# Optimization experiments

Hardware: AMD Instinct MI355X
Metric: run time of the kernel (lower is better)

## Reference

```python
import jax, jax.numpy as jnp
import numpy as np

B = 262144
G = 21       # number of groups (hardcoded in the torch forward)
GS = 8       # features per group
BASIC = 13   # data[:, :13]
H = 512      # hidden_dim
OUT = 1      # output_size


def setup_inputs() -> dict:
    key = jax.random.key(0)
    k0, k1, k2, k3, k4, k5, k6 = jax.random.split(key, 7)
    data = jax.random.normal(k0, (B, BASIC + G * GS), dtype=jnp.float32)
    # per-group Linear(GS, 1): stacked weights [G, GS] and biases [G]
    gW = jax.random.normal(k1, (G, GS), dtype=jnp.float32) * 0.1
    gb = jax.random.normal(k2, (G,), dtype=jnp.float32) * 0.1
    W1 = jax.random.normal(k3, (BASIC + G, H), dtype=jnp.float32) * 0.1
    b1 = jax.random.normal(k4, (H,), dtype=jnp.float32) * 0.1
    W2 = jax.random.normal(k5, (H, OUT), dtype=jnp.float32) * 0.1
    b2 = jax.random.normal(k6, (OUT,), dtype=jnp.float32) * 0.1
    return {"data": data, "gW": gW, "gb": gb, "W1": W1, "b1": b1, "W2": W2, "b2": b2}


def reference(data, gW, gb, W1, b1, W2, b2):
    # Groups are the contiguous, exclusive column slices 13:181 -> [B, G, GS].
    grouped = data[:, BASIC:].reshape(data.shape[0], G, GS)
    # 21 tiny Linear(GS,1)+Sigmoid ops, fused into one batched contraction.
    gout = jax.nn.sigmoid(jnp.einsum("bgd,gd->bg", grouped, gW) + gb)  # [B, G]
    mixed = jnp.concatenate([data[:, :BASIC], gout], axis=1)           # [B, 13+21]
    h = jax.nn.relu(mixed @ W1 + b1)                                   # [B, H]
    return jax.nn.sigmoid(h @ W2 + b2)                                 # [B, OUT]
```

## Files before the change

kernel.cpp:

```cpp
#include <hip/hip_runtime.h>
#include <hip/hip_bf16.h>


#define B_ROWS 262144
#define DFEAT  181
#define BASICF 13
#define NG     21
#define MIXF   34
#define HID    512
#define NT     512
#define TILE   128
#define ROWS_PER_BLOCK 512
#define NTILES (ROWS_PER_BLOCK / TILE)
#define NBLK   (B_ROWS / ROWS_PER_BLOCK)

typedef __attribute__((ext_vector_type(8))) short short8;
typedef __attribute__((ext_vector_type(4))) float float4_t;

__device__ __forceinline__ short f2bf(float f) {
    union { float f; unsigned u; } v; v.f = f;
    unsigned r = (v.u + 0x7FFFu + ((v.u >> 16) & 1u)) >> 16;
    return (short)r;
}
__device__ __forceinline__ float sigm(float x) { return 1.0f / (1.0f + __expf(-x)); }

__global__ __launch_bounds__(NT, 4) void fused_mfma_kernel(
    const float* __restrict__ data, const float* __restrict__ gW,
    const float* __restrict__ gb, const float* __restrict__ W1,
    const float* __restrict__ b1, const float* __restrict__ W2,
    const float* __restrict__ b2, float* __restrict__ out)
{
    __shared__ __align__(16) short   W1f[32 * 64 * 8];
    __shared__ __align__(16) short   mixed[TILE * 32];
    __shared__ __align__(8)  float   mtail[TILE][2];
    __shared__ __align__(16) float4_t wbt[HID];
    __shared__ float gws[NG * 8];
    __shared__ float gbs[NG];

    const int tid = threadIdx.x;

    #pragma unroll 4
    for (int k = 0; k < 32; ++k) {
        int c = tid;
        int t = c >> 4, ci = c & 15;
        int l = ((k >> 3) << 4) + ci;
        int j = k & 7;
        W1f[(t * 64 + l) * 8 + j] = f2bf(W1[k * HID + c]);
    }
    {
        int c = tid;
        wbt[c] = (float4_t){ b1[c], W2[c], W1[32 * HID + c], W1[33 * HID + c] };
    }
    if (tid < NG * 8) gws[tid] = gW[tid];
    if (tid < NG)     gbs[tid] = gb[tid];
    __syncthreads();

    const int wave = tid >> 6;
    const int lane = tid & 63;
    const int lg   = lane >> 4;
    const int li   = lane & 15;
    const float b2v = b2[0];
    const int blk_row0 = blockIdx.x * ROWS_PER_BLOCK;

    {
        const int row0 = blk_row0;
        for (int it = 0; it < 9; ++it) {
            int u = tid + it * NT;
            if (u < TILE * MIXF) {
                int row = u / MIXF, c = u - row * MIXF;
                const float* dr = data + (size_t)(row0 + row) * DFEAT;
                if (c < BASICF) {
                    mixed[row * 32 + c] = f2bf(dr[c]);
                } else {
                    int g = c - BASICF;
                    const float* x = dr + BASICF + g * 8;
                    float s = gbs[g];
                    #pragma unroll
                    for (int k = 0; k < 8; ++k) s = fmaf(x[k], gws[g * 8 + k], s);
                    float v = sigm(s);
                    if (c < 32) mixed[row * 32 + c] = f2bf(v);
                    else        mtail[row][c - 32] = v;
                }
            }
        }
    }
    __syncthreads();

    for (int tile = 0; tile < NTILES; ++tile) {
        const int trow0 = blk_row0 + tile * TILE;

        short8 a0 = *(const short8*)&mixed[(wave * 16 + li) * 32 + lg * 8];
        float2 mt[4];
        #pragma unroll
        for (int j = 0; j < 4; ++j)
            mt[j] = *(const float2*)&mtail[wave * 16 + lg * 4 + j][0];
        __syncthreads();

        if (tile + 1 < NTILES) {
            const int row0 = trow0 + TILE;
            for (int it = 0; it < 9; ++it) {
                int u = tid + it * NT;
                if (u < TILE * MIXF) {
                    int row = u / MIXF, c = u - row * MIXF;
                    const float* dr = data + (size_t)(row0 + row) * DFEAT;
                    if (c < BASICF) {
                        mixed[row * 32 + c] = f2bf(dr[c]);
                    } else {
                        int g = c - BASICF;
                        const float* x = dr + BASICF + g * 8;
                        float s = gbs[g];
                        #pragma unroll
                        for (int k = 0; k < 8; ++k) s = fmaf(x[k], gws[g * 8 + k], s);
                        float v = sigm(s);
                        if (c < 32) mixed[row * 32 + c] = f2bf(v);
                        else        mtail[row][c - 32] = v;
                    }
                }
            }
        }

        float4_t acc = {0.f, 0.f, 0.f, 0.f};
        for (int t = 0; t < 32; ++t) {
            short8 bf = *(const short8*)&W1f[(t * 64 + lane) * 8];
            float4_t c4 = {0.f, 0.f, 0.f, 0.f};
            c4 = __builtin_amdgcn_mfma_f32_16x16x32_bf16(a0, bf, c4, 0, 0, 0);
            int c = t * 16 + li;
            float4_t wv = wbt[c];
            #pragma unroll
            for (int j = 0; j < 4; ++j) {
                float h = c4[j] + wv.x;
                h = fmaf(mt[j].x, wv.z, h);
                h = fmaf(mt[j].y, wv.w, h);
                h = fmaxf(h, 0.f);
                acc[j] = fmaf(h, wv.y, acc[j]);
            }
        }
        #pragma unroll
        for (int m = 1; m < 16; m <<= 1) {
            #pragma unroll
            for (int j = 0; j < 4; ++j) acc[j] += __shfl_xor(acc[j], m, 64);
        }
        if (li == 0) {
            #pragma unroll
            for (int j = 0; j < 4; ++j)
                out[trow0 + wave * 16 + lg * 4 + j] = sigm(acc[j] + b2v);
        }
        __syncthreads();
    }
}

extern "C" void kernel_launch(void* const* d_in, const int* in_sizes, int n_in,
                              void* d_out, int out_size, void* d_ws, size_t ws_size,
                              hipStream_t stream) {
    (void)in_sizes; (void)n_in; (void)out_size; (void)d_ws; (void)ws_size;
    const float* data = (const float*)d_in[0];
    const float* gW   = (const float*)d_in[1];
    const float* gb   = (const float*)d_in[2];
    const float* W1   = (const float*)d_in[3];
    const float* b1   = (const float*)d_in[4];
    const float* W2   = (const float*)d_in[5];
    const float* b2   = (const float*)d_in[6];
    float* out = (float*)d_out;
    fused_mfma_kernel<<<dim3(NBLK), dim3(NT), 0, stream>>>(data, gW, gb, W1, b1, W2, b2, out);
}
```

Before: 51.66 us.

## Split fused kernel into feature-build and MLP kernels via workspace

Splits the single fused kernel into two. The first computes the bf16 mixed features and the fp32 tail into a global workspace with a grid-stride loop, and the second runs the MFMA MLP reading from that workspace. This removes the per-tile block barriers and the in-kernel producer/consumer staging through shared memory. In exchange it adds a global round trip for the intermediate (about 17 MB written and read) and a second launch, and the MLP blocks each still rebuild the W1 fragment table.

Measured after the change: 96.21 us. 1.86x slower.

```diff
diff --git a/kernel.cpp b/kernel.cpp
--- a/kernel.cpp
+++ b/kernel.cpp
@@ -8,11 +8,6 @@
 #define NG     21
 #define MIXF   34
 #define HID    512
-#define NT     512
-#define TILE   128
-#define ROWS_PER_BLOCK 512
-#define NTILES (ROWS_PER_BLOCK / TILE)
-#define NBLK   (B_ROWS / ROWS_PER_BLOCK)
 
 typedef __attribute__((ext_vector_type(8))) short short8;
 typedef __attribute__((ext_vector_type(4))) float float4_t;
@@ -24,35 +19,59 @@
 }
 __device__ __forceinline__ float sigm(float x) { return 1.0f / (1.0f + __expf(-x)); }
 
-__global__ __launch_bounds__(NT, 4) void fused_mfma_kernel(
+#define BUILD_BLOCKS 2048
+__global__ __launch_bounds__(256) void build_kernel(
     const float* __restrict__ data, const float* __restrict__ gW,
-    const float* __restrict__ gb, const float* __restrict__ W1,
-    const float* __restrict__ b1, const float* __restrict__ W2,
-    const float* __restrict__ b2, float* __restrict__ out)
+    const float* __restrict__ gb, short* __restrict__ mixed_g,
+    float* __restrict__ tail_g)
+{
+    __shared__ float gws[NG * 8];
+    __shared__ float gbs[NG];
+    if (threadIdx.x < NG * 8) gws[threadIdx.x] = gW[threadIdx.x];
+    if (threadIdx.x < NG)     gbs[threadIdx.x] = gb[threadIdx.x];
+    __syncthreads();
+
+    const int total  = B_ROWS * MIXF;
+    const int stride = BUILD_BLOCKS * 256;
+    for (int u = blockIdx.x * 256 + threadIdx.x; u < total; u += stride) {
+        int row = u / MIXF;
+        int c   = u - row * MIXF;
+        const float* dr = data + (size_t)row * DFEAT;
+        if (c < BASICF) {
+            mixed_g[row * 32 + c] = f2bf(dr[c]);
+        } else {
+            int g = c - BASICF;
+            const float* x = dr + BASICF + g * 8;
+            float s = gbs[g];
+            #pragma unroll
+            for (int k = 0; k < 8; ++k) s = fmaf(x[k], gws[g * 8 + k], s);
+            float v = sigm(s);
+            if (c < 32) mixed_g[row * 32 + c] = f2bf(v);
+            else        tail_g[row * 2 + (c - 32)] = v;
+        }
+    }
+}
+
+#define MLP_BLOCKS 1024
+__global__ __launch_bounds__(256) void mlp_kernel(
+    const short* __restrict__ mixed_g, const float* __restrict__ tail_g,
+    const float* __restrict__ W1, const float* __restrict__ b1,
+    const float* __restrict__ W2, const float* __restrict__ b2,
+    float* __restrict__ out)
 {
     __shared__ __align__(16) short   W1f[32 * 64 * 8];
-    __shared__ __align__(16) short   mixed[TILE * 32];
-    __shared__ __align__(8)  float   mtail[TILE][2];
     __shared__ __align__(16) float4_t wbt[HID];
-    __shared__ float gws[NG * 8];
-    __shared__ float gbs[NG];
 
     const int tid = threadIdx.x;
-
-    #pragma unroll 4
-    for (int k = 0; k < 32; ++k) {
-        int c = tid;
+    for (int idx = tid; idx < 32 * HID; idx += 256) {
+        int k = idx >> 9, c = idx & 511;
         int t = c >> 4, ci = c & 15;
         int l = ((k >> 3) << 4) + ci;
         int j = k & 7;
         W1f[(t * 64 + l) * 8 + j] = f2bf(W1[k * HID + c]);
     }
-    {
-        int c = tid;
+    for (int c = tid; c < HID; c += 256)
         wbt[c] = (float4_t){ b1[c], W2[c], W1[32 * HID + c], W1[33 * HID + c] };
-    }
-    if (tid < NG * 8) gws[tid] = gW[tid];
-    if (tid < NG)     gbs[tid] = gb[tid];
     __syncthreads();
 
     const int wave = tid >> 6;
@@ -60,64 +79,17 @@
     const int lg   = lane >> 4;
     const int li   = lane & 15;
     const float b2v = b2[0];
-    const int blk_row0 = blockIdx.x * ROWS_PER_BLOCK;
 
-    {
-        const int row0 = blk_row0;
-        for (int it = 0; it < 9; ++it) {
-            int u = tid + it * NT;
-            if (u < TILE * MIXF) {
-                int row = u / MIXF, c = u - row * MIXF;
-                const float* dr = data + (size_t)(row0 + row) * DFEAT;
-                if (c < BASICF) {
-                    mixed[row * 32 + c] = f2bf(dr[c]);
-                } else {
-                    int g = c - BASICF;
-                    const float* x = dr + BASICF + g * 8;
-                    float s = gbs[g];
-                    #pragma unroll
-                    for (int k = 0; k < 8; ++k) s = fmaf(x[k], gws[g * 8 + k], s);
-                    float v = sigm(s);
-                    if (c < 32) mixed[row * 32 + c] = f2bf(v);
-                    else        mtail[row][c - 32] = v;
-                }
-            }
-        }
-    }
-    __syncthreads();
+    #pragma unroll 1
+    for (int it = 0; it < 4; ++it) {
+        const int task = (blockIdx.x * 4 + wave) * 4 + it;
+        const int row0 = task * 16;
 
-    for (int tile = 0; tile < NTILES; ++tile) {
-        const int trow0 = blk_row0 + tile * TILE;
-
-        short8 a0 = *(const short8*)&mixed[(wave * 16 + li) * 32 + lg * 8];
+        short8 a0 = *(const short8*)&mixed_g[(row0 + li) * 32 + lg * 8];
         float2 mt[4];
         #pragma unroll
         for (int j = 0; j < 4; ++j)
-            mt[j] = *(const float2*)&mtail[wave * 16 + lg * 4 + j][0];
-        __syncthreads();
-
-        if (tile + 1 < NTILES) {
-            const int row0 = trow0 + TILE;
-            for (int it = 0; it < 9; ++it) {
-                int u = tid + it * NT;
-                if (u < TILE * MIXF) {
-                    int row = u / MIXF, c = u - row * MIXF;
-                    const float* dr = data + (size_t)(row0 + row) * DFEAT;
-                    if (c < BASICF) {
-                        mixed[row * 32 + c] = f2bf(dr[c]);
-                    } else {
-                        int g = c - BASICF;
-                        const float* x = dr + BASICF + g * 8;
-                        float s = gbs[g];
-                        #pragma unroll
-                        for (int k = 0; k < 8; ++k) s = fmaf(x[k], gws[g * 8 + k], s);
-                        float v = sigm(s);
-                        if (c < 32) mixed[row * 32 + c] = f2bf(v);
-                        else        mtail[row][c - 32] = v;
-                    }
-                }
-            }
-        }
+            mt[j] = *(const float2*)&tail_g[(row0 + lg * 4 + j) * 2];
 
         float4_t acc = {0.f, 0.f, 0.f, 0.f};
         for (int t = 0; t < 32; ++t) {
@@ -143,16 +115,15 @@
         if (li == 0) {
             #pragma unroll
             for (int j = 0; j < 4; ++j)
-                out[trow0 + wave * 16 + lg * 4 + j] = sigm(acc[j] + b2v);
+                out[row0 + lg * 4 + j] = sigm(acc[j] + b2v);
         }
-        __syncthreads();
     }
 }
 
 extern "C" void kernel_launch(void* const* d_in, const int* in_sizes, int n_in,
                               void* d_out, int out_size, void* d_ws, size_t ws_size,
                               hipStream_t stream) {
-    (void)in_sizes; (void)n_in; (void)out_size; (void)d_ws; (void)ws_size;
+    (void)in_sizes; (void)n_in; (void)out_size; (void)ws_size;
     const float* data = (const float*)d_in[0];
     const float* gW   = (const float*)d_in[1];
     const float* gb   = (const float*)d_in[2];
@@ -161,5 +132,10 @@
     const float* W2   = (const float*)d_in[5];
     const float* b2   = (const float*)d_in[6];
     float* out = (float*)d_out;
-    fused_mfma_kernel<<<dim3(NBLK), dim3(NT), 0, stream>>>(data, gW, gb, W1, b1, W2, b2, out);
+
+    short* mixed_g = (short*)d_ws;
+    float* tail_g  = (float*)((char*)d_ws + (size_t)B_ROWS * 32 * 2);
+
+    build_kernel<<<dim3(BUILD_BLOCKS), dim3(256), 0, stream>>>(data, gW, gb, mixed_g, tail_g);
+    mlp_kernel<<<dim3(MLP_BLOCKS), dim3(256), 0, stream>>>(mixed_g, tail_g, W1, b1, W2, b2, out);
 }
```

## Fold bias and tail features into a second MFMA and halve rows per block

Applied to the files above, without the earlier changes.

Bias b1 and the two leftover mixed features are packed into a second bf16 MFMA operand, using a constant-one column for the bias. This removes the per-element scalar FMAs from the hidden-layer epilogue. Rows per block drop from 512 to 256 and the occupancy hint rises from 4 to 6, giving more blocks and waves. The W1 staging loop is rewritten to stride by thread. The tail features and bias are now rounded to bf16, which loses some precision, and the smaller blocks mean W1 is loaded into LDS more often.

Result: slower. 89.87 us (+74.0%).

```diff
diff --git a/kernel.cpp b/kernel.cpp
--- a/kernel.cpp
+++ b/kernel.cpp
@@ -10,7 +10,7 @@
 #define HID    512
 #define NT     512
 #define TILE   128
-#define ROWS_PER_BLOCK 512
+#define ROWS_PER_BLOCK 256
 #define NTILES (ROWS_PER_BLOCK / TILE)
 #define NBLK   (B_ROWS / ROWS_PER_BLOCK)
 
@@ -24,24 +24,24 @@
 }
 __device__ __forceinline__ float sigm(float x) { return 1.0f / (1.0f + __expf(-x)); }
 
-__global__ __launch_bounds__(NT, 4) void fused_mfma_kernel(
+__global__ __launch_bounds__(NT, 6) void fused_mfma_kernel(
     const float* __restrict__ data, const float* __restrict__ gW,
     const float* __restrict__ gb, const float* __restrict__ W1,
     const float* __restrict__ b1, const float* __restrict__ W2,
     const float* __restrict__ b2, float* __restrict__ out)
 {
-    __shared__ __align__(16) short   W1f[32 * 64 * 8];
-    __shared__ __align__(16) short   mixed[TILE * 32];
-    __shared__ __align__(8)  float   mtail[TILE][2];
-    __shared__ __align__(16) float4_t wbt[HID];
+    __shared__ __align__(16) short W1f[32 * 64 * 8];
+    __shared__ __align__(16) short B2f[32 * 16 * 8];
+    __shared__ float W2s[HID];
+    __shared__ __align__(16) short mixed[TILE * 32];
+    __shared__ __align__(8)  short mtailb[TILE * 4];
     __shared__ float gws[NG * 8];
     __shared__ float gbs[NG];
 
     const int tid = threadIdx.x;
 
-    #pragma unroll 4
-    for (int k = 0; k < 32; ++k) {
-        int c = tid;
+    for (int idx = tid; idx < 32 * HID; idx += NT) {
+        int k = idx >> 9, c = idx & 511;
         int t = c >> 4, ci = c & 15;
         int l = ((k >> 3) << 4) + ci;
         int j = k & 7;
@@ -49,8 +49,15 @@
     }
     {
         int c = tid;
-        wbt[c] = (float4_t){ b1[c], W2[c], W1[32 * HID + c], W1[33 * HID + c] };
+        int t = c >> 4, ci = c & 15;
+        short8 v = {0, 0, 0, 0, 0, 0, 0, 0};
+        v[0] = f2bf(W1[32 * HID + c]);
+        v[1] = f2bf(W1[33 * HID + c]);
+        v[2] = f2bf(b1[c]);
+        *(short8*)&B2f[(t * 16 + ci) * 8] = v;
+        W2s[c] = W2[c];
     }
+    if (tid < TILE) ((int*)mtailb)[tid * 2 + 1] = 0x00003F80;
     if (tid < NG * 8) gws[tid] = gW[tid];
     if (tid < NG)     gbs[tid] = gb[tid];
     __syncthreads();
@@ -79,7 +86,7 @@
                     for (int k = 0; k < 8; ++k) s = fmaf(x[k], gws[g * 8 + k], s);
                     float v = sigm(s);
                     if (c < 32) mixed[row * 32 + c] = f2bf(v);
-                    else        mtail[row][c - 32] = v;
+                    else        mtailb[row * 4 + (c - 32)] = f2bf(v);
                 }
             }
         }
@@ -90,10 +97,15 @@
         const int trow0 = blk_row0 + tile * TILE;
 
         short8 a0 = *(const short8*)&mixed[(wave * 16 + li) * 32 + lg * 8];
-        float2 mt[4];
-        #pragma unroll
-        for (int j = 0; j < 4; ++j)
-            mt[j] = *(const float2*)&mtail[wave * 16 + lg * 4 + j][0];
+        short8 a2;
+        {
+            union { int i[4]; short8 s; } ua;
+            const int* mp = (const int*)&mtailb[(wave * 16 + li) * 4];
+            ua.i[0] = (lg == 0) ? mp[0] : 0;
+            ua.i[1] = (lg == 0) ? mp[1] : 0;
+            ua.i[2] = 0; ua.i[3] = 0;
+            a2 = ua.s;
+        }
         __syncthreads();
 
         if (tile + 1 < NTILES) {
@@ -113,7 +125,7 @@
                         for (int k = 0; k < 8; ++k) s = fmaf(x[k], gws[g * 8 + k], s);
                         float v = sigm(s);
                         if (c < 32) mixed[row * 32 + c] = f2bf(v);
-                        else        mtail[row][c - 32] = v;
+                        else        mtailb[row * 4 + (c - 32)] = f2bf(v);
                     }
                 }
             }
@@ -121,18 +133,15 @@
 
         float4_t acc = {0.f, 0.f, 0.f, 0.f};
         for (int t = 0; t < 32; ++t) {
-            short8 bf = *(const short8*)&W1f[(t * 64 + lane) * 8];
+            short8 bf2 = *(const short8*)&B2f[(t * 16 + li) * 8];
+            short8 bf  = *(const short8*)&W1f[(t * 64 + lane) * 8];
             float4_t c4 = {0.f, 0.f, 0.f, 0.f};
-            c4 = __builtin_amdgcn_mfma_f32_16x16x32_bf16(a0, bf, c4, 0, 0, 0);
-            int c = t * 16 + li;
-            float4_t wv = wbt[c];
+            c4 = __builtin_amdgcn_mfma_f32_16x16x32_bf16(a2, bf2, c4, 0, 0, 0);
+            c4 = __builtin_amdgcn_mfma_f32_16x16x32_bf16(a0, bf,  c4, 0, 0, 0);
+            float w2 = W2s[t * 16 + li];
             #pragma unroll
             for (int j = 0; j < 4; ++j) {
-                float h = c4[j] + wv.x;
-                h = fmaf(mt[j].x, wv.z, h);
-                h = fmaf(mt[j].y, wv.w, h);
-                h = fmaxf(h, 0.f);
-                acc[j] = fmaf(h, wv.y, acc[j]);
+                acc[j] = fmaf(fmaxf(c4[j], 0.f), w2, acc[j]);
             }
         }
         #pragma unroll
```

## Keep W1 fragments in registers and swap MFMA roles with double-buffered tiles

Applied to the files above, without the earlier changes.

Each wave now holds its 64-column slice of W1 as bf16 MFMA A-fragments in registers, replacing the shared-memory W1 copy. Row tiles become the B operand. The two tail features and b1 are folded into a second MFMA using a constant-1 column. Tiles are double-buffered with a padded stride to cut the extra barrier and bank conflicts. Per-wave partial dot products go through shared memory and 128 threads reduce them. This removes the per-iteration LDS weight reads and scalar bias/tail FMAs, at the cost of more registers, bf16 rounding of the tail features and b1, and an extra barrier per tile.

Result: slower. 78.23 us (+51.4%).

```diff
diff --git a/kernel.cpp b/kernel.cpp
--- a/kernel.cpp
+++ b/kernel.cpp
@@ -10,6 +10,7 @@
 #define HID    512
 #define NT     512
 #define TILE   128
+#define MSTRIDE 40
 #define ROWS_PER_BLOCK 512
 #define NTILES (ROWS_PER_BLOCK / TILE)
 #define NBLK   (B_ROWS / ROWS_PER_BLOCK)
@@ -24,43 +25,58 @@
 }
 __device__ __forceinline__ float sigm(float x) { return 1.0f / (1.0f + __expf(-x)); }
 
-__global__ __launch_bounds__(NT, 4) void fused_mfma_kernel(
+__global__ __launch_bounds__(NT) void fused_mfma_kernel(
     const float* __restrict__ data, const float* __restrict__ gW,
     const float* __restrict__ gb, const float* __restrict__ W1,
     const float* __restrict__ b1, const float* __restrict__ W2,
     const float* __restrict__ b2, float* __restrict__ out)
 {
-    __shared__ __align__(16) short   W1f[32 * 64 * 8];
-    __shared__ __align__(16) short   mixed[TILE * 32];
-    __shared__ __align__(8)  float   mtail[TILE][2];
-    __shared__ __align__(16) float4_t wbt[HID];
+    __shared__ __align__(16) short mixed[2][TILE * MSTRIDE];
+    __shared__ short mtailb[2][TILE * 2];
+    __shared__ float partials[8][TILE];
     __shared__ float gws[NG * 8];
     __shared__ float gbs[NG];
 
-    const int tid = threadIdx.x;
-
-    #pragma unroll 4
-    for (int k = 0; k < 32; ++k) {
-        int c = tid;
-        int t = c >> 4, ci = c & 15;
-        int l = ((k >> 3) << 4) + ci;
-        int j = k & 7;
-        W1f[(t * 64 + l) * 8 + j] = f2bf(W1[k * HID + c]);
-    }
-    {
-        int c = tid;
-        wbt[c] = (float4_t){ b1[c], W2[c], W1[32 * HID + c], W1[33 * HID + c] };
-    }
-    if (tid < NG * 8) gws[tid] = gW[tid];
-    if (tid < NG)     gbs[tid] = gb[tid];
-    __syncthreads();
-
+    const int tid  = threadIdx.x;
     const int wave = tid >> 6;
     const int lane = tid & 63;
     const int lg   = lane >> 4;
     const int li   = lane & 15;
+
+    if (tid < NG * 8) gws[tid] = gW[tid];
+    if (tid < NG)     gbs[tid] = gb[tid];
+
+    const int c0 = wave * 64;
+    short8 aW[4];
+    #pragma unroll
+    for (int s = 0; s < 4; ++s) {
+        int c = c0 + s * 16 + li;
+        #pragma unroll
+        for (int j = 0; j < 8; ++j)
+            aW[s][j] = f2bf(W1[(lg * 8 + j) * HID + c]);
+    }
+    short8 a2[4];
+    #pragma unroll
+    for (int s = 0; s < 4; ++s) {
+        int c = c0 + s * 16 + li;
+        short8 v = {0, 0, 0, 0, 0, 0, 0, 0};
+        if (lg == 0) {
+            v[0] = f2bf(W1[32 * HID + c]);
+            v[1] = f2bf(W1[33 * HID + c]);
+            v[2] = f2bf(b1[c]);
+        }
+        a2[s] = v;
+    }
+    float w2r[4][4];
+    #pragma unroll
+    for (int s = 0; s < 4; ++s)
+        #pragma unroll
+        for (int j = 0; j < 4; ++j)
+            w2r[s][j] = W2[c0 + s * 16 + lg * 4 + j];
+
     const float b2v = b2[0];
     const int blk_row0 = blockIdx.x * ROWS_PER_BLOCK;
+    __syncthreads();
 
     {
         const int row0 = blk_row0;
@@ -70,7 +86,7 @@
                 int row = u / MIXF, c = u - row * MIXF;
                 const float* dr = data + (size_t)(row0 + row) * DFEAT;
                 if (c < BASICF) {
-                    mixed[row * 32 + c] = f2bf(dr[c]);
+                    mixed[0][row * MSTRIDE + c] = f2bf(dr[c]);
                 } else {
                     int g = c - BASICF;
                     const float* x = dr + BASICF + g * 8;
@@ -78,33 +94,28 @@
                     #pragma unroll
                     for (int k = 0; k < 8; ++k) s = fmaf(x[k], gws[g * 8 + k], s);
                     float v = sigm(s);
-                    if (c < 32) mixed[row * 32 + c] = f2bf(v);
-                    else        mtail[row][c - 32] = v;
+                    if (c < 32) mixed[0][row * MSTRIDE + c] = f2bf(v);
+                    else        mtailb[0][row * 2 + (c - 32)] = f2bf(v);
                 }
             }
         }
     }
     __syncthreads();
 
+    int cur = 0;
     for (int tile = 0; tile < NTILES; ++tile) {
         const int trow0 = blk_row0 + tile * TILE;
 
-        short8 a0 = *(const short8*)&mixed[(wave * 16 + li) * 32 + lg * 8];
-        float2 mt[4];
-        #pragma unroll
-        for (int j = 0; j < 4; ++j)
-            mt[j] = *(const float2*)&mtail[wave * 16 + lg * 4 + j][0];
-        __syncthreads();
-
         if (tile + 1 < NTILES) {
             const int row0 = trow0 + TILE;
+            const int nb = cur ^ 1;
             for (int it = 0; it < 9; ++it) {
                 int u = tid + it * NT;
                 if (u < TILE * MIXF) {
                     int row = u / MIXF, c = u - row * MIXF;
                     const float* dr = data + (size_t)(row0 + row) * DFEAT;
                     if (c < BASICF) {
-                        mixed[row * 32 + c] = f2bf(dr[c]);
+                        mixed[nb][row * MSTRIDE + c] = f2bf(dr[c]);
                     } else {
                         int g = c - BASICF;
                         const float* x = dr + BASICF + g * 8;
@@ -112,40 +123,51 @@
                         #pragma unroll
                         for (int k = 0; k < 8; ++k) s = fmaf(x[k], gws[g * 8 + k], s);
                         float v = sigm(s);
-                        if (c < 32) mixed[row * 32 + c] = f2bf(v);
-                        else        mtail[row][c - 32] = v;
+                        if (c < 32) mixed[nb][row * MSTRIDE + c] = f2bf(v);
+                        else        mtailb[nb][row * 2 + (c - 32)] = f2bf(v);
                     }
                 }
             }
         }
 
-        float4_t acc = {0.f, 0.f, 0.f, 0.f};
-        for (int t = 0; t < 32; ++t) {
-            short8 bf = *(const short8*)&W1f[(t * 64 + lane) * 8];
-            float4_t c4 = {0.f, 0.f, 0.f, 0.f};
-            c4 = __builtin_amdgcn_mfma_f32_16x16x32_bf16(a0, bf, c4, 0, 0, 0);
-            int c = t * 16 + li;
-            float4_t wv = wbt[c];
+        for (int task = 0; task < 8; ++task) {
+            short8 bfrag = *(const short8*)&mixed[cur][(task * 16 + li) * MSTRIDE + lg * 8];
+            short8 b2f;
+            {
+                union { int i[4]; short8 s8; } ub;
+                int mv = *(const int*)&mtailb[cur][(task * 16 + li) * 2];
+                ub.i[0] = (lg == 0) ? mv : 0;
+                ub.i[1] = (lg == 0) ? 0x00003F80 : 0;
+                ub.i[2] = 0; ub.i[3] = 0;
+                b2f = ub.s8;
+            }
+            float4_t z = {0.f, 0.f, 0.f, 0.f};
+            float4_t c4[4];
             #pragma unroll
-            for (int j = 0; j < 4; ++j) {
-                float h = c4[j] + wv.x;
-                h = fmaf(mt[j].x, wv.z, h);
-                h = fmaf(mt[j].y, wv.w, h);
-                h = fmaxf(h, 0.f);
-                acc[j] = fmaf(h, wv.y, acc[j]);
-            }
-        }
-        #pragma unroll
-        for (int m = 1; m < 16; m <<= 1) {
+            for (int s = 0; s < 4; ++s)
+                c4[s] = __builtin_amdgcn_mfma_f32_16x16x32_bf16(a2[s], b2f, z, 0, 0, 0);
             #pragma unroll
-            for (int j = 0; j < 4; ++j) acc[j] += __shfl_xor(acc[j], m, 64);
-        }
-        if (li == 0) {
+            for (int s = 0; s < 4; ++s)
+                c4[s] = __builtin_amdgcn_mfma_f32_16x16x32_bf16(aW[s], bfrag, c4[s], 0, 0, 0);
+            float p = 0.f;
             #pragma unroll
-            for (int j = 0; j < 4; ++j)
-                out[trow0 + wave * 16 + lg * 4 + j] = sigm(acc[j] + b2v);
+            for (int s = 0; s < 4; ++s)
+                #pragma unroll
+                for (int j = 0; j < 4; ++j)
+                    p = fmaf(fmaxf(c4[s][j], 0.f), w2r[s][j], p);
+            p += __shfl_xor(p, 16, 64);
+            p += __shfl_xor(p, 32, 64);
+            if (lane < 16) partials[wave][task * 16 + lane] = p;
         }
         __syncthreads();
+
+        if (tid < TILE) {
+            float s = partials[0][tid] + partials[1][tid] + partials[2][tid] + partials[3][tid]
+                    + partials[4][tid] + partials[5][tid] + partials[6][tid] + partials[7][tid];
+            out[trow0 + tid] = sigm(s + b2v);
+        }
+        __syncthreads();
+        cur ^= 1;
     }
 }
 
```
